# Optimization experiments

Measured on AMD Instinct MI355X. Metric: run time of the kernel, lower is better.

## Reference

```python
import jax, jax.numpy as jnp
import numpy as np

N, E = 20000, 320000          # nodes, edges
R, B = 9, 9                   # num_relations, num_bases
IN, HID, OUT = 128, 256, 64   # feature dims
EPS = 1e-5                    # LayerNorm eps


def layer_norm(h, gamma, beta):
    mu = jnp.mean(h, axis=-1, keepdims=True)
    var = jnp.var(h, axis=-1, keepdims=True)
    return (h - mu) * jax.lax.rsqrt(var + EPS) * gamma + beta


def rgcn_conv(x, src, dst, etype, bases, comp, root, bias, aggr):
    # basis decomposition: W_r = sum_b comp[r,b] * bases[b]
    W = jnp.einsum('rb,bio->rio', comp, bases)          # [R, in, out]
    xW = jnp.einsum('ni,rio->rno', x, W)                # [R, N, out]
    msg = xW[etype, src]                                # [E, out] gather per edge
    if aggr == 'max':
        agg = jax.ops.segment_max(msg, dst, num_segments=N)
        agg = jnp.where(jnp.isfinite(agg), agg, 0.0)    # empty segments -> 0
    else:
        agg = jax.ops.segment_sum(msg, dst, num_segments=N)
    return agg + x @ root + bias


def setup_inputs() -> dict:
    key = jax.random.key(0)
    ks = jax.random.split(key, 12)
    rn = lambda k, s, sc=0.05: jax.random.normal(k, s, jnp.float32) * sc
    return {
        'x': jax.random.normal(ks[0], (N, IN), jnp.float32),
        'edge_index': jax.random.randint(ks[1], (2, E), 0, N),
        'edge_type': jax.random.randint(ks[2], (E,), 0, R),
        # conv1 params
        'bases1': rn(ks[3], (B, IN, HID)),
        'comp1': rn(ks[4], (R, B), 0.3),
        'root1': rn(ks[5], (IN, HID)),
        'bias1': jnp.zeros((HID,), jnp.float32),
        'g1': jnp.ones((HID,), jnp.float32),
        'b1': jnp.zeros((HID,), jnp.float32),
        # conv2 params
        'bases2': rn(ks[6], (B, HID, OUT)),
        'comp2': rn(ks[7], (R, B), 0.3),
        'root2': rn(ks[8], (HID, OUT)),
        'bias2': jnp.zeros((OUT,), jnp.float32),
        'g2': jnp.ones((OUT,), jnp.float32),
        'b2': jnp.zeros((OUT,), jnp.float32),
    }


def reference(x, edge_index, edge_type, bases1, comp1, root1, bias1, g1, b1,
              bases2, comp2, root2, bias2, g2, b2):
    src, dst = edge_index[0], edge_index[1]
    h = rgcn_conv(x, src, dst, edge_type, bases1, comp1, root1, bias1, 'max')
    h = jax.nn.relu(layer_norm(h, g1, b1))
    # eval mode: edge dropout and feature dropout are identity
    h = rgcn_conv(h, src, dst, edge_type, bases2, comp2, root2, bias2, 'add')
    h = layer_norm(h, g2, b2)
    return jax.nn.log_softmax(h, axis=1)
```

## Files before the change

kernel.cpp:

```cpp
#include <hip/hip_runtime.h>
#include <math.h>

#define NN 20000
#define NE 320000
#define NREL 9
#define NBASES 9
#define D_IN 128
#define D_HID 256
#define D_OUT 64
#define LN_EPS 1e-5f

#define N1 (NREL * D_HID + D_HID)
#define N2 (NREL * D_OUT + D_OUT)
#define NBLK ((NN + 255) / 256)

#define LSTR 40

typedef __attribute__((ext_vector_type(8))) short bf16x8;
typedef __attribute__((ext_vector_type(4))) float f32x4;

__device__ inline ushort f2b(float f) {
    unsigned u = __float_as_uint(f);
    return (ushort)((u + 0x7FFFu + ((u >> 16) & 1u)) >> 16);
}
__device__ inline float b2f(ushort h) { return __uint_as_float(((unsigned)h) << 16); }
__device__ inline unsigned pack2bf(float f0, float f1) {
    return (unsigned)f2b(f0) | ((unsigned)f2b(f1) << 16);
}

__global__ __launch_bounds__(256) void prep_all(
    const float* __restrict__ bases1, const float* __restrict__ comp1, const float* __restrict__ root1,
    const float* __restrict__ bases2, const float* __restrict__ comp2, const float* __restrict__ root2,
    const float* __restrict__ x,
    ushort* __restrict__ w1t, ushort* __restrict__ w2t, ushort* __restrict__ xbf)
{
    const int SZ1 = N1 * D_IN;
    const int SZ2 = N2 * D_HID;
    const int SZX = NN * D_IN;
    int tid = blockIdx.x * 256 + threadIdx.x;
    if (tid < SZ1) {
        int n = tid >> 7, k = tid & 127;
        float s;
        if (n < NREL * D_HID) {
            int r = n >> 8, o = n & 255;
            s = 0.f;
            #pragma unroll
            for (int b = 0; b < NBASES; b++)
                s += comp1[r * NBASES + b] * bases1[(b * D_IN + k) * D_HID + o];
        } else {
            s = root1[k * D_HID + (n - NREL * D_HID)];
        }
        w1t[tid] = f2b(s);
    } else if (tid < SZ1 + SZ2) {
        int j = tid - SZ1;
        int n = j >> 8, k = j & 255;
        float s;
        if (n < NREL * D_OUT) {
            int r = n >> 6, o = n & 63;
            s = 0.f;
            #pragma unroll
            for (int b = 0; b < NBASES; b++)
                s += comp2[r * NBASES + b] * bases2[(b * D_HID + k) * D_OUT + o];
        } else {
            s = root2[k * D_OUT + (n - NREL * D_OUT)];
        }
        w2t[j] = f2b(s);
    } else if (tid < SZ1 + SZ2 + SZX) {
        int j = tid - SZ1 - SZ2;
        xbf[j] = f2b(x[j]);
    }
}

__global__ __launch_bounds__(256) void hist_dst(const int* __restrict__ dst, int* __restrict__ deg)
{
    int e = blockIdx.x * 256 + threadIdx.x;
    if (e < NE) atomicAdd(&deg[dst[e]], 1);
}

__global__ __launch_bounds__(256) void scan_blk(
    const int* __restrict__ deg, int* __restrict__ local, int* __restrict__ bsum)
{
    __shared__ int wsum[4];
    int tid = threadIdx.x, lane = tid & 63, w = tid >> 6;
    int i = blockIdx.x * 256 + tid;
    int v = (i < NN) ? deg[i] : 0;
    int x = v;
    #pragma unroll
    for (int d = 1; d < 64; d <<= 1) {
        int y = __shfl_up(x, d, 64);
        if (lane >= d) x += y;
    }
    if (lane == 63) wsum[w] = x;
    __syncthreads();
    int woff = 0;
    for (int j = 0; j < w; j++) woff += wsum[j];
    if (i < NN) local[i] = woff + x - v;
    if (tid == 255) bsum[blockIdx.x] = woff + x;
}

__global__ __launch_bounds__(64) void scan_top(const int* __restrict__ bsum, int* __restrict__ boff)
{
    int lane = threadIdx.x;
    int carry = 0;
    for (int base = 0; base < NBLK; base += 64) {
        int i = base + lane;
        int v = (i < NBLK) ? bsum[i] : 0;
        int x = v;
        #pragma unroll
        for (int d = 1; d < 64; d <<= 1) {
            int y = __shfl_up(x, d, 64);
            if (lane >= d) x += y;
        }
        if (i < NBLK) boff[i] = carry + x - v;
        carry += __shfl(x, 63, 64);
    }
}

__global__ __launch_bounds__(256) void scan_fin(
    const int* __restrict__ local, const int* __restrict__ boff,
    int* __restrict__ offs, int* __restrict__ cursor)
{
    int i = blockIdx.x * 256 + threadIdx.x;
    if (i < NN) {
        int o = local[i] + boff[i >> 8];
        offs[i] = o;
        cursor[i] = o;
    }
    if (i == NN) offs[NN] = NE;
}

__global__ __launch_bounds__(256) void scatter_ep(
    const int* __restrict__ src, const int* __restrict__ dst, const int* __restrict__ etype,
    int* __restrict__ cursor, int* __restrict__ ep1, int* __restrict__ ep2)
{
    int e = blockIdx.x * 256 + threadIdx.x;
    if (e >= NE) return;
    int d = dst[e];
    int s = src[e], r = etype[e];
    int pos = atomicAdd(&cursor[d], 1);
    ep1[pos] = s * N1 + r * D_HID;
    ep2[pos] = s * N2 + r * D_OUT;
}

__global__ __launch_bounds__(256) void gemm_bf16(
    const ushort* __restrict__ A, const ushort* __restrict__ Bt, ushort* __restrict__ C,
    int M, int N, int K)
{
    __shared__ ushort As[2][128 * LSTR];
    __shared__ ushort Bs[2][128 * LSTR];

    int tid = threadIdx.x;
    int lane = tid & 63, w = tid >> 6;
    int wm = w >> 1, wn = w & 1;
    int row0 = blockIdx.y * 128, col0 = blockIdx.x * 128;

    int r0 = tid >> 2, q0 = tid & 3;
    int arow0 = min(row0 + r0, M - 1);
    int arow1 = min(row0 + r0 + 64, M - 1);
    const ushort* gA0 = &A[(size_t)arow0 * K + q0 * 8];
    const ushort* gA1 = &A[(size_t)arow1 * K + q0 * 8];
    const ushort* gB0 = &Bt[(size_t)(col0 + r0) * K + q0 * 8];
    const ushort* gB1 = &Bt[(size_t)(col0 + r0 + 64) * K + q0 * 8];
    int lo0 = r0 * LSTR + q0 * 8;
    int lo1 = (r0 + 64) * LSTR + q0 * 8;

    f32x4 acc[4][4];
    #pragma unroll
    for (int mt = 0; mt < 4; mt++)
        #pragma unroll
        for (int nt = 0; nt < 4; nt++)
            acc[mt][nt] = (f32x4){0.f, 0.f, 0.f, 0.f};

    {
        bf16x8 a0 = *(const bf16x8*)gA0;
        bf16x8 a1 = *(const bf16x8*)gA1;
        bf16x8 b0 = *(const bf16x8*)gB0;
        bf16x8 b1 = *(const bf16x8*)gB1;
        *(bf16x8*)&As[0][lo0] = a0;
        *(bf16x8*)&As[0][lo1] = a1;
        *(bf16x8*)&Bs[0][lo0] = b0;
        *(bf16x8*)&Bs[0][lo1] = b1;
    }

    int mr = lane & 15, kq = lane >> 4;
    const int NC = K >> 5;
    for (int c = 0; c < NC; c++) {
        __syncthreads();
        int cur = c & 1, nxt = cur ^ 1;
        bf16x8 a0, a1, b0, b1;
        bool more = (c + 1 < NC);
        if (more) {
            gA0 += 32; gA1 += 32; gB0 += 32; gB1 += 32;
            a0 = *(const bf16x8*)gA0;
            a1 = *(const bf16x8*)gA1;
            b0 = *(const bf16x8*)gB0;
            b1 = *(const bf16x8*)gB1;
        }

        bf16x8 af[4], bfr[4];
        #pragma unroll
        for (int mt = 0; mt < 4; mt++)
            af[mt] = *(const bf16x8*)&As[cur][(wm * 64 + mt * 16 + mr) * LSTR + kq * 8];
        #pragma unroll
        for (int nt = 0; nt < 4; nt++)
            bfr[nt] = *(const bf16x8*)&Bs[cur][(wn * 64 + nt * 16 + mr) * LSTR + kq * 8];
        #pragma unroll
        for (int mt = 0; mt < 4; mt++)
            #pragma unroll
            for (int nt = 0; nt < 4; nt++)
                acc[mt][nt] = __builtin_amdgcn_mfma_f32_16x16x32_bf16(
                    bfr[nt], af[mt], acc[mt][nt], 0, 0, 0);

        if (more) {
            *(bf16x8*)&As[nxt][lo0] = a0;
            *(bf16x8*)&As[nxt][lo1] = a1;
            *(bf16x8*)&Bs[nxt][lo0] = b0;
            *(bf16x8*)&Bs[nxt][lo1] = b1;
        }
    }

    int q = lane >> 4, cm = lane & 15;
    #pragma unroll
    for (int mt = 0; mt < 4; mt++) {
        int gr = row0 + wm * 64 + mt * 16 + cm;
        if (gr < M) {
            #pragma unroll
            for (int nt = 0; nt < 4; nt++) {
                int gc = col0 + wn * 64 + nt * 16 + q * 4;
                uint2 o;
                o.x = pack2bf(acc[mt][nt][0], acc[mt][nt][1]);
                o.y = pack2bf(acc[mt][nt][2], acc[mt][nt][3]);
                *(uint2*)&C[(size_t)gr * N + gc] = o;
            }
        }
    }
}

__global__ __launch_bounds__(256) void gather1(
    const ushort* __restrict__ xw1, const int* __restrict__ offs, const int* __restrict__ ep1,
    const float* __restrict__ bias, const float* __restrict__ g, const float* __restrict__ b,
    ushort* __restrict__ h)
{
    int n = blockIdx.x * 4 + (threadIdx.x >> 6);
    if (n >= NN) return;
    int lane = threadIdx.x & 63;
    int lane4 = lane * 4;
    int e0 = __builtin_amdgcn_readfirstlane(offs[n]);
    int e1 = __builtin_amdgcn_readfirstlane(offs[n + 1]);

    float m0 = -INFINITY, m1 = -INFINITY, m2 = -INFINITY, m3 = -INFINITY;
    int e = e0;
    for (; e + 8 <= e1; e += 8) {
        int p[8];
        #pragma unroll
        for (int j = 0; j < 8; j++) p[j] = ep1[e + j];
        ushort4 v[8];
        #pragma unroll
        for (int j = 0; j < 8; j++) v[j] = *(const ushort4*)&xw1[(size_t)(p[j] + lane4)];
        #pragma unroll
        for (int j = 0; j < 8; j++) {
            m0 = fmaxf(m0, b2f(v[j].x)); m1 = fmaxf(m1, b2f(v[j].y));
            m2 = fmaxf(m2, b2f(v[j].z)); m3 = fmaxf(m3, b2f(v[j].w));
        }
    }
    for (; e + 2 <= e1; e += 2) {
        int pa = ep1[e], pb = ep1[e + 1];
        ushort4 va = *(const ushort4*)&xw1[(size_t)(pa + lane4)];
        ushort4 vb = *(const ushort4*)&xw1[(size_t)(pb + lane4)];
        m0 = fmaxf(m0, fmaxf(b2f(va.x), b2f(vb.x)));
        m1 = fmaxf(m1, fmaxf(b2f(va.y), b2f(vb.y)));
        m2 = fmaxf(m2, fmaxf(b2f(va.z), b2f(vb.z)));
        m3 = fmaxf(m3, fmaxf(b2f(va.w), b2f(vb.w)));
    }
    for (; e < e1; e++) {
        int p = ep1[e];
        ushort4 v = *(const ushort4*)&xw1[(size_t)(p + lane4)];
        m0 = fmaxf(m0, b2f(v.x)); m1 = fmaxf(m1, b2f(v.y));
        m2 = fmaxf(m2, b2f(v.z)); m3 = fmaxf(m3, b2f(v.w));
    }
    if (e1 == e0) { m0 = m1 = m2 = m3 = 0.f; }

    ushort4 rt = *(const ushort4*)&xw1[(size_t)n * N1 + NREL * D_HID + lane4];
    int c = lane4;
    float t0 = m0 + b2f(rt.x) + bias[c + 0];
    float t1 = m1 + b2f(rt.y) + bias[c + 1];
    float t2 = m2 + b2f(rt.z) + bias[c + 2];
    float t3 = m3 + b2f(rt.w) + bias[c + 3];

    float s = t0 + t1 + t2 + t3;
    float s2 = t0 * t0 + t1 * t1 + t2 * t2 + t3 * t3;
    #pragma unroll
    for (int m = 32; m >= 1; m >>= 1) {
        s  += __shfl_xor(s,  m, 64);
        s2 += __shfl_xor(s2, m, 64);
    }
    float mu = s * (1.f / D_HID);
    float var = s2 * (1.f / D_HID) - mu * mu;
    float rs = rsqrtf(var + LN_EPS);

    ushort4 o;
    o.x = f2b(fmaxf((t0 - mu) * rs * g[c + 0] + b[c + 0], 0.f));
    o.y = f2b(fmaxf((t1 - mu) * rs * g[c + 1] + b[c + 1], 0.f));
    o.z = f2b(fmaxf((t2 - mu) * rs * g[c + 2] + b[c + 2], 0.f));
    o.w = f2b(fmaxf((t3 - mu) * rs * g[c + 3] + b[c + 3], 0.f));
    *(ushort4*)&h[(size_t)n * D_HID + c] = o;
}

__global__ __launch_bounds__(256) void gather2(
    const ushort* __restrict__ xw2, const int* __restrict__ offs, const int* __restrict__ ep2,
    const float* __restrict__ bias, const float* __restrict__ g, const float* __restrict__ b,
    float* __restrict__ out)
{
    int n = blockIdx.x * 4 + (threadIdx.x >> 6);
    if (n >= NN) return;
    int lane = threadIdx.x & 63;
    int e0 = __builtin_amdgcn_readfirstlane(offs[n]);
    int e1 = __builtin_amdgcn_readfirstlane(offs[n + 1]);

    float s = 0.f;
    int e = e0;
    for (; e + 4 <= e1; e += 4) {
        int p0 = ep2[e + 0], p1 = ep2[e + 1], p2 = ep2[e + 2], p3 = ep2[e + 3];
        float a0 = b2f(xw2[(size_t)(p0 + lane)]);
        float a1 = b2f(xw2[(size_t)(p1 + lane)]);
        float a2 = b2f(xw2[(size_t)(p2 + lane)]);
        float a3 = b2f(xw2[(size_t)(p3 + lane)]);
        s += (a0 + a1) + (a2 + a3);
    }
    for (; e < e1; e++) {
        s += b2f(xw2[(size_t)(ep2[e] + lane)]);
    }
    float v = s + b2f(xw2[(size_t)n * N2 + NREL * D_OUT + lane]) + bias[lane];

    float sm = v, s2 = v * v;
    #pragma unroll
    for (int m = 32; m >= 1; m >>= 1) {
        sm += __shfl_xor(sm, m, 64);
        s2 += __shfl_xor(s2, m, 64);
    }
    float mu = sm * (1.f / D_OUT);
    float var = s2 * (1.f / D_OUT) - mu * mu;
    float y = (v - mu) * rsqrtf(var + LN_EPS) * g[lane] + b[lane];

    float mx = y;
    #pragma unroll
    for (int m = 32; m >= 1; m >>= 1) mx = fmaxf(mx, __shfl_xor(mx, m, 64));
    float ex = __expf(y - mx);
    float se = ex;
    #pragma unroll
    for (int m = 32; m >= 1; m >>= 1) se += __shfl_xor(se, m, 64);
    out[(size_t)n * D_OUT + lane] = y - mx - logf(se);
}

extern "C" void kernel_launch(void* const* d_in, const int* in_sizes, int n_in,
                              void* d_out, int out_size, void* d_ws, size_t ws_size,
                              hipStream_t stream)
{
    const float* x      = (const float*)d_in[0];
    const int*   eidx   = (const int*)  d_in[1];
    const int*   etype  = (const int*)  d_in[2];
    const float* bases1 = (const float*)d_in[3];
    const float* comp1  = (const float*)d_in[4];
    const float* root1  = (const float*)d_in[5];
    const float* bias1  = (const float*)d_in[6];
    const float* g1     = (const float*)d_in[7];
    const float* b1     = (const float*)d_in[8];
    const float* bases2 = (const float*)d_in[9];
    const float* comp2  = (const float*)d_in[10];
    const float* root2  = (const float*)d_in[11];
    const float* bias2  = (const float*)d_in[12];
    const float* g2     = (const float*)d_in[13];
    const float* b2     = (const float*)d_in[14];

    const int* src = eidx;
    const int* dst = eidx + NE;

    char* p = (char*)d_ws;
    auto alloc = [&](size_t bytes) -> char* {
        char* r = p;
        p += (bytes + 255) & ~(size_t)255;
        return r;
    };
    ushort* xbf    = (ushort*)alloc((size_t)NN * D_IN * 2);
    ushort* w1t    = (ushort*)alloc((size_t)N1 * D_IN * 2);
    ushort* w2t    = (ushort*)alloc((size_t)N2 * D_HID * 2);
    ushort* xw1    = (ushort*)alloc((size_t)NN * N1 * 2);
    ushort* xw2    = (ushort*)alloc((size_t)NN * N2 * 2);
    ushort* h      = (ushort*)alloc((size_t)NN * D_HID * 2);
    int*    deg    = (int*)   alloc((size_t)NN * 4);
    int*    local  = (int*)   alloc((size_t)NN * 4);
    int*    bsum   = (int*)   alloc((size_t)NBLK * 4);
    int*    boff   = (int*)   alloc((size_t)NBLK * 4);
    int*    offs   = (int*)   alloc((size_t)(NN + 1) * 4);
    int*    cursor = (int*)   alloc((size_t)NN * 4);
    int*    ep1    = (int*)   alloc((size_t)NE * 4);
    int*    ep2    = (int*)   alloc((size_t)NE * 4);

    const int SZP = N1 * D_IN + N2 * D_HID + NN * D_IN;
    prep_all<<<(SZP + 255) / 256, 256, 0, stream>>>(
        bases1, comp1, root1, bases2, comp2, root2, x, w1t, w2t, xbf);

    hipMemsetAsync(deg, 0, (size_t)NN * 4, stream);
    hist_dst<<<(NE + 255) / 256, 256, 0, stream>>>(dst, deg);
    scan_blk<<<NBLK, 256, 0, stream>>>(deg, local, bsum);
    scan_top<<<1, 64, 0, stream>>>(bsum, boff);
    scan_fin<<<NBLK, 256, 0, stream>>>(local, boff, offs, cursor);
    scatter_ep<<<(NE + 255) / 256, 256, 0, stream>>>(src, dst, etype, cursor, ep1, ep2);

    gemm_bf16<<<dim3(N1 / 128, (NN + 127) / 128), 256, 0, stream>>>(xbf, w1t, xw1, NN, N1, D_IN);
    gather1<<<(NN + 3) / 4, 256, 0, stream>>>(xw1, offs, ep1, bias1, g1, b1, h);

    gemm_bf16<<<dim3(N2 / 128, (NN + 127) / 128), 256, 0, stream>>>(h, w2t, xw2, NN, N2, D_HID);
    gather2<<<(NN + 3) / 4, 256, 0, stream>>>(xw2, offs, ep2, bias2, g2, b2, (float*)d_out);
}
```

Baseline: 256.6 us.

## Store GEMM LDS tiles in MFMA fragment order and fold top-level scan into scan_fin

```diff
diff --git a/kernel.cpp b/kernel.cpp
--- a/kernel.cpp
+++ b/kernel.cpp
@@ -13,8 +13,6 @@
 #define N1 (NREL * D_HID + D_HID)
 #define N2 (NREL * D_OUT + D_OUT)
 #define NBLK ((NN + 255) / 256)
-
-#define LSTR 40
 
 typedef __attribute__((ext_vector_type(8))) short bf16x8;
 typedef __attribute__((ext_vector_type(4))) float f32x4;
@@ -98,31 +96,31 @@
     if (tid == 255) bsum[blockIdx.x] = woff + x;
 }
 
-__global__ __launch_bounds__(64) void scan_top(const int* __restrict__ bsum, int* __restrict__ boff)
-{
-    int lane = threadIdx.x;
-    int carry = 0;
-    for (int base = 0; base < NBLK; base += 64) {
-        int i = base + lane;
-        int v = (i < NBLK) ? bsum[i] : 0;
-        int x = v;
-        #pragma unroll
-        for (int d = 1; d < 64; d <<= 1) {
-            int y = __shfl_up(x, d, 64);
-            if (lane >= d) x += y;
-        }
-        if (i < NBLK) boff[i] = carry + x - v;
-        carry += __shfl(x, 63, 64);
-    }
-}
-
 __global__ __launch_bounds__(256) void scan_fin(
-    const int* __restrict__ local, const int* __restrict__ boff,
+    const int* __restrict__ local, const int* __restrict__ bsum,
     int* __restrict__ offs, int* __restrict__ cursor)
 {
-    int i = blockIdx.x * 256 + threadIdx.x;
+    __shared__ int boff_s[NBLK];
+    int tid = threadIdx.x;
+    if (tid < 64) {
+        int carry = 0;
+        for (int base = 0; base < NBLK; base += 64) {
+            int i = base + tid;
+            int v = (i < NBLK) ? bsum[i] : 0;
+            int x = v;
+            #pragma unroll
+            for (int d = 1; d < 64; d <<= 1) {
+                int y = __shfl_up(x, d, 64);
+                if (tid >= d) x += y;
+            }
+            if (i < NBLK) boff_s[i] = carry + x - v;
+            carry += __shfl(x, 63, 64);
+        }
+    }
+    __syncthreads();
+    int i = blockIdx.x * 256 + tid;
     if (i < NN) {
-        int o = local[i] + boff[i >> 8];
+        int o = local[i] + boff_s[i >> 8];
         offs[i] = o;
         cursor[i] = o;
     }
@@ -146,23 +144,23 @@
     const ushort* __restrict__ A, const ushort* __restrict__ Bt, ushort* __restrict__ C,
     int M, int N, int K)
 {
-    __shared__ ushort As[2][128 * LSTR];
-    __shared__ ushort Bs[2][128 * LSTR];
+    __shared__ ushort As[2][512 * 8];
+    __shared__ ushort Bs[2][512 * 8];
 
     int tid = threadIdx.x;
     int lane = tid & 63, w = tid >> 6;
     int wm = w >> 1, wn = w & 1;
     int row0 = blockIdx.y * 128, col0 = blockIdx.x * 128;
 
-    int r0 = tid >> 2, q0 = tid & 3;
-    int arow0 = min(row0 + r0, M - 1);
-    int arow1 = min(row0 + r0 + 64, M - 1);
-    const ushort* gA0 = &A[(size_t)arow0 * K + q0 * 8];
-    const ushort* gA1 = &A[(size_t)arow1 * K + q0 * 8];
-    const ushort* gB0 = &Bt[(size_t)(col0 + r0) * K + q0 * 8];
-    const ushort* gB1 = &Bt[(size_t)(col0 + r0 + 64) * K + q0 * 8];
-    int lo0 = r0 * LSTR + q0 * 8;
-    int lo1 = (r0 + 64) * LSTR + q0 * 8;
+    int s0 = tid, s1 = tid + 256;
+    int g0 = s0 >> 6, kc0 = (s0 >> 4) & 3, mr0 = s0 & 15;
+    int g1 = s1 >> 6, kc1 = (s1 >> 4) & 3, mr1 = s1 & 15;
+    int arow0 = min(row0 + g0 * 16 + mr0, M - 1);
+    int arow1 = min(row0 + g1 * 16 + mr1, M - 1);
+    const ushort* gA0 = &A[(size_t)arow0 * K + kc0 * 8];
+    const ushort* gA1 = &A[(size_t)arow1 * K + kc1 * 8];
+    const ushort* gB0 = &Bt[(size_t)(col0 + g0 * 16 + mr0) * K + kc0 * 8];
+    const ushort* gB1 = &Bt[(size_t)(col0 + g1 * 16 + mr1) * K + kc1 * 8];
 
     f32x4 acc[4][4];
     #pragma unroll
@@ -176,13 +174,12 @@
         bf16x8 a1 = *(const bf16x8*)gA1;
         bf16x8 b0 = *(const bf16x8*)gB0;
         bf16x8 b1 = *(const bf16x8*)gB1;
-        *(bf16x8*)&As[0][lo0] = a0;
-        *(bf16x8*)&As[0][lo1] = a1;
-        *(bf16x8*)&Bs[0][lo0] = b0;
-        *(bf16x8*)&Bs[0][lo1] = b1;
-    }
-
-    int mr = lane & 15, kq = lane >> 4;
+        *(bf16x8*)&As[0][s0 * 8] = a0;
+        *(bf16x8*)&As[0][s1 * 8] = a1;
+        *(bf16x8*)&Bs[0][s0 * 8] = b0;
+        *(bf16x8*)&Bs[0][s1 * 8] = b1;
+    }
+
     const int NC = K >> 5;
     for (int c = 0; c < NC; c++) {
         __syncthreads();
@@ -200,10 +197,10 @@
         bf16x8 af[4], bfr[4];
         #pragma unroll
         for (int mt = 0; mt < 4; mt++)
-            af[mt] = *(const bf16x8*)&As[cur][(wm * 64 + mt * 16 + mr) * LSTR + kq * 8];
+            af[mt] = *(const bf16x8*)&As[cur][(size_t)(((wm * 4 + mt) * 64) + lane) * 8];
         #pragma unroll
         for (int nt = 0; nt < 4; nt++)
-            bfr[nt] = *(const bf16x8*)&Bs[cur][(wn * 64 + nt * 16 + mr) * LSTR + kq * 8];
+            bfr[nt] = *(const bf16x8*)&Bs[cur][(size_t)(((wn * 4 + nt) * 64) + lane) * 8];
         #pragma unroll
         for (int mt = 0; mt < 4; mt++)
             #pragma unroll
@@ -212,10 +209,10 @@
                     bfr[nt], af[mt], acc[mt][nt], 0, 0, 0);
 
         if (more) {
-            *(bf16x8*)&As[nxt][lo0] = a0;
-            *(bf16x8*)&As[nxt][lo1] = a1;
-            *(bf16x8*)&Bs[nxt][lo0] = b0;
-            *(bf16x8*)&Bs[nxt][lo1] = b1;
+            *(bf16x8*)&As[nxt][s0 * 8] = a0;
+            *(bf16x8*)&As[nxt][s1 * 8] = a1;
+            *(bf16x8*)&Bs[nxt][s0 * 8] = b0;
+            *(bf16x8*)&Bs[nxt][s1 * 8] = b1;
         }
     }
 
@@ -390,7 +387,6 @@
     int*    deg    = (int*)   alloc((size_t)NN * 4);
     int*    local  = (int*)   alloc((size_t)NN * 4);
     int*    bsum   = (int*)   alloc((size_t)NBLK * 4);
-    int*    boff   = (int*)   alloc((size_t)NBLK * 4);
     int*    offs   = (int*)   alloc((size_t)(NN + 1) * 4);
     int*    cursor = (int*)   alloc((size_t)NN * 4);
     int*    ep1    = (int*)   alloc((size_t)NE * 4);
@@ -403,8 +399,7 @@
     hipMemsetAsync(deg, 0, (size_t)NN * 4, stream);
     hist_dst<<<(NE + 255) / 256, 256, 0, stream>>>(dst, deg);
     scan_blk<<<NBLK, 256, 0, stream>>>(deg, local, bsum);
-    scan_top<<<1, 64, 0, stream>>>(bsum, boff);
-    scan_fin<<<NBLK, 256, 0, stream>>>(local, boff, offs, cursor);
+    scan_fin<<<NBLK, 256, 0, stream>>>(local, bsum, offs, cursor);
     scatter_ep<<<(NE + 255) / 256, 256, 0, stream>>>(src, dst, etype, cursor, ep1, ep2);
 
     gemm_bf16<<<dim3(N1 / 128, (NN + 127) / 128), 256, 0, stream>>>(xbf, w1t, xw1, NN, N1, D_IN);
```

After: 268.3 us. +4.6%, slower.
